# Kernel tuning notes

Measured on AMD Instinct MI355X. Metric: run time of the kernel, lower is better.

Reference implementation:

```python
import jax, jax.numpy as jnp
import numpy as np

B, N, T, D, E, M = 8, 512, 64, 128, 32, 3


def _norm(v):
    return v / jnp.clip(jnp.linalg.norm(v, axis=-1, keepdims=True), 1e-12)


def setup_inputs() -> dict:
    key = jax.random.key(0)
    ks = jax.random.split(key, 14)
    s = 0.05
    x = jax.random.normal(ks[0], (B, N, T, 1), jnp.float32)
    # set_prior: binarized adjacency + self loops, row-normalized
    a = (jax.random.uniform(ks[1], (N, N)) > 0.95).astype(jnp.float32) + jnp.eye(N, dtype=jnp.float32)
    prior = a / jnp.clip(a.sum(1, keepdims=True), 1e-8)
    # orthogonal queries, as in torch __init__ (QR of zero-padded randn)
    rng = np.random.default_rng(0)
    qs = []
    for _ in range(M):
        pad = np.zeros((D, D), np.float32)
        pad[:E] = rng.standard_normal((E, D)).astype(np.float32) * 0.1
        q, _ = np.linalg.qr(pad)
        qs.append(q[:E])
    return {
        "x": x,
        "prior": prior,
        "proj_W": jax.random.normal(ks[2], (D, 1), jnp.float32) * s,
        "proj_b": jnp.zeros((D,), jnp.float32),
        "W_ih": jax.random.normal(ks[3], (3 * D, D), jnp.float32) * s,
        "W_hh": jax.random.normal(ks[4], (3 * D, D), jnp.float32) * s,
        "b_ih": jnp.zeros((3 * D,), jnp.float32),
        "b_hh": jnp.zeros((3 * D,), jnp.float32),
        "space_W": jax.random.normal(ks[5], (M, D, D), jnp.float32) * s,
        "space_b": jnp.zeros((M, D), jnp.float32),
        "router_W": jax.random.normal(ks[6], (M, 2 * D), jnp.float32) * s,
        "router_b": jnp.zeros((M,), jnp.float32),
        "out_W": jax.random.normal(ks[7], (1, D), jnp.float32) * s,
        "out_b": jnp.zeros((1,), jnp.float32),
        "prior_logit": jnp.array(1.0, jnp.float32),
        "queries": jnp.asarray(np.stack(qs)),  # [M, E, D]
    }


def reference(x, prior, proj_W, proj_b, W_ih, W_hh, b_ih, b_hh,
              space_W, space_b, router_W, router_b, out_W, out_b,
              prior_logit, queries):
    b, n, t, _ = x.shape
    d = proj_b.shape[0]
    m, e, _ = queries.shape
    # proj(x.permute(0,2,1,3)).reshape(B*N, T, D)  (faithful reshape of [B,T,N,D])
    hp = jnp.transpose(x, (0, 2, 1, 3)) @ proj_W.T + proj_b  # [B,T,N,D]
    seq = hp.reshape(b * n, t, d)
    xs = jnp.swapaxes(seq, 0, 1)  # [T, BN, D]

    def gru_step(h, xt):
        gi = xt @ W_ih.T + b_ih
        gh = h @ W_hh.T + b_hh
        ir, iz, i_n = jnp.split(gi, 3, axis=-1)
        hr, hz, h_n = jnp.split(gh, 3, axis=-1)
        r = jax.nn.sigmoid(ir + hr)
        z = jax.nn.sigmoid(iz + hz)
        ng = jnp.tanh(i_n + r * h_n)
        return (1.0 - z) * ng + z * h, None

    h, _ = jax.lax.scan(gru_step, jnp.zeros((b * n, d), x.dtype), xs)
    h = h.reshape(b, n, d)

    stats = jnp.concatenate([h.mean(1), jnp.std(h, axis=1, ddof=1)], axis=-1)  # torch std is unbiased
    probs = jax.nn.softmax(stats @ router_W.T + router_b, axis=-1)  # [B,M]

    z_prior = jnp.einsum('ij,bjd->bid', prior, h)

    hs = _norm(jnp.einsum('bnd,mkd->bmnk', h, space_W) + space_b[None, :, None, :])  # [B,M,N,D]
    q = _norm(queries)  # [M,E,D]
    scores = jnp.einsum('bmnd,med->bmen', hs, q)  # [B,M,E,N] (topk over N axis)
    k = min(n, max(4, int(n * 0.05)))
    vals, idx = jax.lax.top_k(scores, k)  # [B,M,E,k]
    w = jax.nn.softmax(vals / 0.7, axis=-1)
    H = jnp.zeros((b, m, e, n), h.dtype).at[
        jnp.arange(b)[:, None, None, None],
        jnp.arange(m)[None, :, None, None],
        jnp.arange(e)[None, None, :, None],
        idx,
    ].set(w)  # [B,M,E,N], transposed layout of torch's [B,N,E]

    Hmix = jnp.einsum('bmen,bm->ben', H, probs)  # [B,E,N] == torch Hmix^T
    edge = jnp.einsum('ben,bnd->bed', Hmix, h)   # Hmix^T @ h
    z_learn = jnp.einsum('ben,bed->bnd', Hmix, edge)  # Hmix @ edge

    alpha = jax.nn.sigmoid(prior_logit)
    out = (alpha * z_prior + (1.0 - alpha) * z_learn) @ out_W.T + out_b  # [B,N,1]
    return out.squeeze(-1), probs
```

## Files before the change

kernel.cpp:

```cpp
#include <hip/hip_runtime.h>
#include <math.h>

#define OFF_U      0
#define OFF_C      384
#define OFF_QWHI   768
#define OFF_QWLO   6912
#define OFF_H      13056
#define OFF_PROBS  537344
#define OFF_HV     537376
#define OFF_SCORES 541472
#define OFF_HMIX   934688
#define OFF_WHI    1066016
#define OFF_SHI    1115168
#define OFF_SLO    1139744
#define OFF_STATS  1164320
#define OFF_EV     1229856
#define OFF_QB     1230112

typedef short bf16x8 __attribute__((ext_vector_type(8)));
typedef float f32x4 __attribute__((ext_vector_type(4)));

union U8 { unsigned short s[8]; bf16x8 v; uint4 u4; };

__device__ __forceinline__ unsigned short bf16_rtn(float f) {
  unsigned int u = __float_as_uint(f);
  return (unsigned short)((u + 0x7FFFu + ((u >> 16) & 1u)) >> 16);
}
__device__ __forceinline__ float bf16_f(unsigned short h) {
  return __uint_as_float(((unsigned int)h) << 16);
}

__global__ __launch_bounds__(256) void prep_kernel(const float* __restrict__ Wih,
                                                   const float* __restrict__ projW,
                                                   const float* __restrict__ projb,
                                                   const float* __restrict__ bih,
                                                   const float* __restrict__ queries,
                                                   const float* __restrict__ Whh,
                                                   const float* __restrict__ spaceW,
                                                   const float* __restrict__ spaceb,
                                                   float* __restrict__ ws) {
  const int bid = blockIdx.x, tid = threadIdx.x;
  const int wave = tid >> 6, lane = tid & 63;
  if (bid < 96) {
    int r = bid * 4 + wave;
    float w0 = Wih[r * 128 + lane], w1 = Wih[r * 128 + 64 + lane];
    float u = w0 * projW[lane] + w1 * projW[64 + lane];
    float c = w0 * projb[lane] + w1 * projb[64 + lane];
    for (int off = 32; off; off >>= 1) {
      u += __shfl_xor(u, off);
      c += __shfl_xor(c, off);
    }
    if (lane == 0) {
      ws[OFF_U + r] = u;
      ws[OFF_C + r] = c + bih[r];
    }
  } else if (bid < 112) {
    unsigned short* WHI = (unsigned short*)(ws + OFF_WHI);
    int base = (bid - 96) * 3072;
    for (int i = tid; i < 3072; i += 256)
      WHI[base + i] = bf16_rtn(Whh[base + i]);
  } else if (bid < 128) {
    unsigned short* SHI = (unsigned short*)(ws + OFF_SHI);
    unsigned short* SLO = (unsigned short*)(ws + OFF_SLO);
    int base = (bid - 112) * 3072;
    for (int i = tid; i < 3072; i += 256) {
      float w = spaceW[base + i];
      unsigned short hi = bf16_rtn(w);
      SHI[base + i] = hi;
      SLO[base + i] = bf16_rtn(w - bf16_f(hi));
    }
  } else if (bid < 224) {
    int qi = bid - 128;
    int m = qi >> 5, e = qi & 31;
    __shared__ float invS, qdS;
    const float* qrow = queries + (m * 32 + e) * 128;
    if (wave == 0) {
      float v0 = qrow[lane], v1 = qrow[64 + lane];
      float ss = v0 * v0 + v1 * v1;
      for (int off = 32; off; off >>= 1) ss += __shfl_xor(ss, off);
      if (lane == 0) invS = 1.f / fmaxf(sqrtf(ss), 1e-12f);
    } else if (wave == 1) {
      float v = qrow[lane] * spaceb[m * 128 + lane] +
                qrow[64 + lane] * spaceb[m * 128 + 64 + lane];
      for (int off = 32; off; off >>= 1) v += __shfl_xor(v, off);
      if (lane == 0) qdS = v;
    }
    __syncthreads();
    if (tid < 128) {
      int din = tid;
      float acc = 0.f;
      for (int dout = 0; dout < 128; ++dout)
        acc += qrow[dout] * spaceW[m * 16384 + dout * 128 + din];
      acc *= invS;
      unsigned short hi = bf16_rtn(acc);
      ((unsigned short*)(ws + OFF_QWHI))[(m * 32 + e) * 128 + din] = hi;
      ((unsigned short*)(ws + OFF_QWLO))[(m * 32 + e) * 128 + din] =
          bf16_rtn(acc - bf16_f(hi));
    }
    if (tid == 255) ws[OFF_QB + m * 32 + e] = qdS * invS;
  } else {
    ws[OFF_EV + tid] = 0.f;
  }
}

__global__ __launch_bounds__(512, 2) void gru_kernel(const float* __restrict__ x,
                                                     const float* __restrict__ bhh,
                                                     const float* __restrict__ outW,
                                                     float* __restrict__ ws) {
  __shared__ __align__(16) unsigned short hB[2][16 * 17 * 8];
  __shared__ float xsAll[16 * 65];
  __shared__ float hFin[16 * 132];

  const int tid = threadIdx.x, wave = tid >> 6, lane = tid & 63;
  const int q = lane >> 4, s15 = lane & 15;
  const int d = wave * 16 + s15;
  const unsigned short* WHI = (const unsigned short*)(ws + OFF_WHI);

  {
    float4 z4 = make_float4(0.f, 0.f, 0.f, 0.f);
    float4* hm4 = (float4*)(ws + OFF_HMIX);
    if (tid < 128) hm4[blockIdx.x * 128 + tid] = z4;
  }

  bf16x8 Bh[3][4];
#pragma unroll
  for (int t = 0; t < 3; ++t) {
    int row = (wave + 8 * t) * 16 + s15;
#pragma unroll
    for (int c = 0; c < 4; ++c)
      Bh[t][c] = *(const bf16x8*)&WHI[row * 128 + c * 32 + q * 8];
  }
  const float ur = ws[OFF_U + d],       uz = ws[OFF_U + 128 + d], un = ws[OFF_U + 256 + d];
  const float cr = ws[OFF_C + d] + bhh[d];
  const float cz = ws[OFF_C + 128 + d] + bhh[128 + d];
  const float cn = ws[OFF_C + 256 + d];
  const float bj2 = bhh[256 + d];

  const int seq0 = blockIdx.x * 16;
  for (int i = tid; i < 1024; i += 512) {
    int s = i >> 6, tt = i & 63;
    int r = (seq0 + s) * 64 + tt;
    xsAll[s * 65 + tt] = x[((r >> 15) * 512 + (r & 511)) * 64 + ((r >> 9) & 63)];
  }
  for (int i = tid; i < 2176; i += 512) hB[0][i] = 0;
  __syncthreads();

  float hreg[4] = {0.f, 0.f, 0.f, 0.f};
  const int g = d >> 3, e = d & 7;

  for (int t = 0; t < 64; ++t) {
    const int rb = t & 1, wb = rb ^ 1;
    f32x4 acc0 = {0.f, 0.f, 0.f, 0.f};
    f32x4 acc1 = {0.f, 0.f, 0.f, 0.f};
    f32x4 acc2 = {0.f, 0.f, 0.f, 0.f};
#pragma unroll
    for (int c = 0; c < 4; ++c) {
      bf16x8 A = *(const bf16x8*)&hB[rb][((c * 4 + q) * 17 + s15) * 8];
      acc0 = __builtin_amdgcn_mfma_f32_16x16x32_bf16(A, Bh[0][c], acc0, 0, 0, 0);
      acc1 = __builtin_amdgcn_mfma_f32_16x16x32_bf16(A, Bh[1][c], acc1, 0, 0, 0);
      acc2 = __builtin_amdgcn_mfma_f32_16x16x32_bf16(A, Bh[2][c], acc2, 0, 0, 0);
    }
    float xsv[4];
#pragma unroll
    for (int r = 0; r < 4; ++r) xsv[r] = xsAll[(q * 4 + r) * 65 + t];
#pragma unroll
    for (int r = 0; r < 4; ++r) {
      int s = q * 4 + r;
      float gr = fmaf(xsv[r], ur, cr + acc0[r]);
      float gz = fmaf(xsv[r], uz, cz + acc1[r]);
      float gn = fmaf(xsv[r], un, cn);
      float hn = acc2[r] + bj2;
      float rr = __builtin_amdgcn_rcpf(1.f + __expf(-gr));
      float zm = __builtin_amdgcn_rcpf(1.f + __expf(gz));
      float a = fmaf(rr, hn, gn);
      float ng = 1.f - 2.f * __builtin_amdgcn_rcpf(__expf(2.f * a) + 1.f);
      float hv = fmaf(zm, ng - hreg[r], hreg[r]);
      hreg[r] = hv;
      hB[wb][(g * 17 + s) * 8 + e] = bf16_rtn(hv);
    }
    __syncthreads();
  }

#pragma unroll
  for (int r = 0; r < 4; ++r) hFin[(q * 4 + r) * 132 + d] = hreg[r];
  __syncthreads();
  float* h_out = ws + OFF_H;
#pragma unroll
  for (int p = 0; p < 4; ++p) {
    int item = tid + p * 512;
    int s = item >> 7, dd = item & 127;
    h_out[(seq0 + s) * 128 + dd] = hFin[s * 132 + dd];
  }
  for (int s = wave * 2; s < wave * 2 + 2; ++s) {
    float a = hFin[s * 132 + lane] * outW[lane] + hFin[s * 132 + 64 + lane] * outW[64 + lane];
    for (int off = 32; off; off >>= 1) a += __shfl_xor(a, off);
    if (lane == 0) ws[OFF_HV + seq0 + s] = a;
  }
  if (tid < 128) {
    float s = 0.f, q2 = 0.f;
#pragma unroll
    for (int sI = 0; sI < 16; ++sI) {
      float v = hFin[sI * 132 + tid];
      s += v; q2 += v * v;
    }
    ws[OFF_STATS + blockIdx.x * 256 + tid] = s;
    ws[OFF_STATS + blockIdx.x * 256 + 128 + tid] = q2;
  }
}

__global__ __launch_bounds__(256) void scores_kernel(const float* __restrict__ spaceb,
                                                     const float* __restrict__ routerW,
                                                     const float* __restrict__ routerb,
                                                     float* __restrict__ ws,
                                                     float* __restrict__ d_out) {
  const int bid = blockIdx.x;
  const int chunk = bid & 15, m = (bid >> 4) % 3, b = bid / 48;
  const int n0 = chunk * 32;
  const int tid = threadIdx.x, wave = tid >> 6, lane = tid & 63;
  const int q = lane >> 4, s15 = lane & 15;

  __shared__ __align__(16) unsigned short sHi[16 * 33 * 8];
  __shared__ __align__(16) unsigned short sLo[16 * 33 * 8];
  __shared__ float hsL[32 * 132];
  __shared__ float biasL[128];
  __shared__ float invnL[32];
  __shared__ float qbL[32];

  const float* hG = ws + OFF_H;
  const unsigned short* SHI = (const unsigned short*)(ws + OFF_SHI);
  const unsigned short* SLO = (const unsigned short*)(ws + OFF_SLO);
  const unsigned short* QWHI = (const unsigned short*)(ws + OFF_QWHI);
  const unsigned short* QWLO = (const unsigned short*)(ws + OFF_QWLO);

  if (tid < 128) biasL[tid] = spaceb[m * 128 + tid];
  else if (tid < 160) qbL[tid - 128] = ws[OFF_QB + m * 32 + (tid - 128)];
  {
    int nn = tid >> 3, kc = tid & 7;
    const float* row = &hG[(b * 512 + n0 + nn) * 128 + kc * 16];
    U8 ph0, pl0, ph1, pl1;
#pragma unroll
    for (int j = 0; j < 8; ++j) {
      float v = row[j];
      unsigned short hi = bf16_rtn(v);
      ph0.s[j] = hi; pl0.s[j] = bf16_rtn(v - bf16_f(hi));
    }
#pragma unroll
    for (int j = 0; j < 8; ++j) {
      float v = row[8 + j];
      unsigned short hi = bf16_rtn(v);
      ph1.s[j] = hi; pl1.s[j] = bf16_rtn(v - bf16_f(hi));
    }
    int g0 = kc * 2;
    *(uint4*)&sHi[(g0 * 33 + nn) * 8] = ph0.u4;
    *(uint4*)&sLo[(g0 * 33 + nn) * 8] = pl0.u4;
    *(uint4*)&sHi[((g0 + 1) * 33 + nn) * 8] = ph1.u4;
    *(uint4*)&sLo[((g0 + 1) * 33 + nn) * 8] = pl1.u4;
  }
  __syncthreads();

  const int nt = wave >> 1;
  const int half = wave & 1;
  const int dt0 = half * 4;
  f32x4 acc[4] = {{0.f,0.f,0.f,0.f},{0.f,0.f,0.f,0.f},{0.f,0.f,0.f,0.f},{0.f,0.f,0.f,0.f}};
  f32x4 accS = {0.f, 0.f, 0.f, 0.f};
#pragma unroll
  for (int c = 0; c < 4; ++c) {
    bf16x8 Ahi = *(const bf16x8*)&sHi[((c * 4 + q) * 33 + nt * 16 + s15) * 8];
    bf16x8 Alo = *(const bf16x8*)&sLo[((c * 4 + q) * 33 + nt * 16 + s15) * 8];
#pragma unroll
    for (int i = 0; i < 4; ++i) {
      int row = m * 16384 + ((dt0 + i) * 16 + s15) * 128 + c * 32 + q * 8;
      bf16x8 Bhi = *(const bf16x8*)&SHI[row];
      bf16x8 Blo = *(const bf16x8*)&SLO[row];
      acc[i] = __builtin_amdgcn_mfma_f32_16x16x32_bf16(Ahi, Bhi, acc[i], 0, 0, 0);
      acc[i] = __builtin_amdgcn_mfma_f32_16x16x32_bf16(Alo, Bhi, acc[i], 0, 0, 0);
      acc[i] = __builtin_amdgcn_mfma_f32_16x16x32_bf16(Ahi, Blo, acc[i], 0, 0, 0);
    }
    {
      int row = (m * 32 + half * 16 + s15) * 128 + c * 32 + q * 8;
      bf16x8 Qhi = *(const bf16x8*)&QWHI[row];
      bf16x8 Qlo = *(const bf16x8*)&QWLO[row];
      accS = __builtin_amdgcn_mfma_f32_16x16x32_bf16(Ahi, Qhi, accS, 0, 0, 0);
      accS = __builtin_amdgcn_mfma_f32_16x16x32_bf16(Alo, Qhi, accS, 0, 0, 0);
      accS = __builtin_amdgcn_mfma_f32_16x16x32_bf16(Ahi, Qlo, accS, 0, 0, 0);
    }
  }
#pragma unroll
  for (int i = 0; i < 4; ++i) {
    int dcol = (dt0 + i) * 16 + s15;
    float bb = biasL[dcol];
#pragma unroll
    for (int r = 0; r < 4; ++r)
      hsL[(nt * 16 + q * 4 + r) * 132 + dcol] = acc[i][r] + bb;
  }
  __syncthreads();

  {
    int n = tid >> 3, kc = tid & 7;
    float ss = 0.f;
#pragma unroll
    for (int d4 = 0; d4 < 4; ++d4) {
      float4 v = *(const float4*)&hsL[n * 132 + kc * 16 + d4 * 4];
      ss += v.x * v.x + v.y * v.y + v.z * v.z + v.w * v.w;
    }
    ss += __shfl_xor(ss, 1); ss += __shfl_xor(ss, 2); ss += __shfl_xor(ss, 4);
    if (kc == 0) invnL[n] = 1.f / fmaxf(sqrtf(ss), 1e-12f);
  }
  __syncthreads();

  {
    int e = half * 16 + s15;
    float qb = qbL[e];
    int nb = nt * 16 + q * 4;
    float4 o;
    o.x = (accS[0] + qb) * invnL[nb + 0];
    o.y = (accS[1] + qb) * invnL[nb + 1];
    o.z = (accS[2] + qb) * invnL[nb + 2];
    o.w = (accS[3] + qb) * invnL[nb + 3];
    *(float4*)&ws[OFF_SCORES + ((b * 3 + m) * 32 + e) * 512 + n0 + nb] = o;
  }

  if ((bid % 48) == 0) {
    __syncthreads();
    float* st = hsL;
    float* lgS = hsL + 256;
    if (tid < 128) {
      float s = 0.f, q2 = 0.f;
      const float* base = ws + OFF_STATS + b * 32 * 256;
      for (int j = 0; j < 32; ++j) {
        s += base[j * 256 + tid];
        q2 += base[j * 256 + 128 + tid];
      }
      float mean = s * (1.f / 512.f);
      float var = (q2 - 512.f * mean * mean) * (1.f / 511.f);
      st[tid] = mean;
      st[128 + tid] = sqrtf(fmaxf(var, 0.f));
    }
    __syncthreads();
    if (tid < 3) {
      float acc2 = routerb[tid];
      for (int k = 0; k < 256; ++k) acc2 += st[k] * routerW[tid * 256 + k];
      lgS[tid] = acc2;
    }
    __syncthreads();
    if (tid == 0) {
      float mx = fmaxf(lgS[0], fmaxf(lgS[1], lgS[2]));
      float e0 = expf(lgS[0] - mx), e1 = expf(lgS[1] - mx), e2 = expf(lgS[2] - mx);
      float inv = 1.f / (e0 + e1 + e2);
      ws[OFF_PROBS + b * 3 + 0] = e0 * inv;
      ws[OFF_PROBS + b * 3 + 1] = e1 * inv;
      ws[OFF_PROBS + b * 3 + 2] = e2 * inv;
      d_out[4096 + b * 3 + 0] = e0 * inv;
      d_out[4096 + b * 3 + 1] = e1 * inv;
      d_out[4096 + b * 3 + 2] = e2 * inv;
    }
  }
}

__global__ __launch_bounds__(256) void topk_kernel(float* __restrict__ ws) {
  const int row0 = blockIdx.x * 4;
  const int b = row0 / 96;
  const int tid = threadIdx.x, wave = tid >> 6, lane = tid & 63;
  __shared__ float hvL[512];
  hvL[tid] = ws[OFF_HV + b * 512 + tid];
  hvL[256 + tid] = ws[OFF_HV + b * 512 + 256 + tid];
  __syncthreads();

  int row = row0 + wave;
  int m = (row / 32) % 3, e = row & 31;
  const float* sc = ws + OFF_SCORES + row * 512;
  float prob = ws[OFF_PROBS + b * 3 + m];

  float v[8];
#pragma unroll
  for (int j = 0; j < 8; ++j) v[j] = sc[j * 64 + lane];

  float selv = 0.f; int seli = 0; float maxv = 0.f;
  for (int it = 0; it < 25; ++it) {
    float bv = v[0]; int bj = 0;
#pragma unroll
    for (int j = 1; j < 8; ++j)
      if (v[j] > bv) { bv = v[j]; bj = j; }
    int bidx = bj * 64 + lane;
    for (int off = 32; off; off >>= 1) {
      float ov = __shfl_xor(bv, off);
      int oi = __shfl_xor(bidx, off);
      if (ov > bv || (ov == bv && oi < bidx)) { bv = ov; bidx = oi; }
    }
    if (lane == (bidx & 63)) v[bidx >> 6] = -INFINITY;
    if (it == 0) maxv = bv;
    if (lane == it) { selv = bv; seli = bidx; }
  }
  float ex = (lane < 25) ? __expf((selv - maxv) * (1.f / 0.7f)) : 0.f;
  float den = ex;
  for (int off = 32; off; off >>= 1) den += __shfl_xor(den, off);
  float w = prob * ex / den;
  if (lane < 25)
    atomicAdd(&ws[OFF_HMIX + (b * 32 + e) * 512 + seli], w);
  float evc = (lane < 25) ? w * hvL[seli] : 0.f;
  for (int off = 32; off; off >>= 1) evc += __shfl_xor(evc, off);
  if (lane == 0) atomicAdd(&ws[OFF_EV + b * 32 + e], evc);
}

__global__ __launch_bounds__(512) void final_kernel(const float* __restrict__ prior,
                                                    const float* __restrict__ outb,
                                                    const float* __restrict__ plog,
                                                    float* __restrict__ ws,
                                                    float* __restrict__ d_out) {
  const int bid = blockIdx.x;
  const int b = bid >> 4, ch = bid & 15;
  const int tid = threadIdx.x, wave = tid >> 6, lane = tid & 63;
  __shared__ float hvL[512], evL[32];
  hvL[tid] = ws[OFF_HV + b * 512 + tid];
  if (tid < 32) evL[tid] = ws[OFF_EV + b * 32 + tid];
  __syncthreads();
  float alpha = 1.f / (1.f + expf(-plog[0]));
  float ob = outb[0];
#pragma unroll
  for (int i = 0; i < 4; ++i) {
    int n = ch * 32 + wave * 4 + i;
    const float* pr = prior + n * 512;
    float s1 = 0.f;
#pragma unroll
    for (int j = 0; j < 8; ++j) s1 += pr[j * 64 + lane] * hvL[j * 64 + lane];
    float s2 = 0.f;
    if (lane < 32) s2 = ws[OFF_HMIX + (b * 32 + lane) * 512 + n] * evL[lane];
    float a = alpha * s1 + (1.f - alpha) * s2;
    for (int off = 32; off; off >>= 1) a += __shfl_xor(a, off);
    if (lane == 0) d_out[b * 512 + n] = a + ob;
  }
}

extern "C" void kernel_launch(void* const* d_in, const int* in_sizes, int n_in,
                              void* d_out, int out_size, void* d_ws, size_t ws_size,
                              hipStream_t stream) {
  const float* x       = (const float*)d_in[0];
  const float* prior   = (const float*)d_in[1];
  const float* projW   = (const float*)d_in[2];
  const float* projb   = (const float*)d_in[3];
  const float* Wih     = (const float*)d_in[4];
  const float* Whh     = (const float*)d_in[5];
  const float* bih     = (const float*)d_in[6];
  const float* bhh     = (const float*)d_in[7];
  const float* spaceW  = (const float*)d_in[8];
  const float* spaceb  = (const float*)d_in[9];
  const float* routerW = (const float*)d_in[10];
  const float* routerb = (const float*)d_in[11];
  const float* outW    = (const float*)d_in[12];
  const float* outb    = (const float*)d_in[13];
  const float* plog    = (const float*)d_in[14];
  const float* queries = (const float*)d_in[15];
  float* ws  = (float*)d_ws;
  float* out = (float*)d_out;

  prep_kernel<<<225, 256, 0, stream>>>(Wih, projW, projb, bih, queries, Whh,
                                       spaceW, spaceb, ws);
  gru_kernel<<<256, 512, 0, stream>>>(x, bhh, outW, ws);
  scores_kernel<<<384, 256, 0, stream>>>(spaceb, routerW, routerb, ws, out);
  topk_kernel<<<192, 256, 0, stream>>>(ws);
  final_kernel<<<128, 512, 0, stream>>>(prior, outb, plog, ws, out);
}
```

Measured before the change: 177.7 us.

## Transpose GRU MFMA operands, fold log2e into weights, pack bf16 stores

The GRU step now puts the recurrent weights in the A operand and the hidden state in the B operand. Each lane therefore owns four consecutive hidden dims of one sequence, and the x input is a single scalar per lane. The log2(e) scaling is folded into W_hh and the gate constants during prep, so the gates use raw exp2 and the biases start in the accumulator. New h values are packed with v_cvt_pk_bf16_f32 and written as one 8-byte LDS store. The loop is manually unrolled by two to make the buffer indices compile-time constants. Together these cut per-step VALU work, LDS store count and address arithmetic on the serial 64-step critical path. The cost is a slightly different rounding, since W_hh is scaled before the bf16 conversion.

After: 167.1 us. 6.0% less time.

```diff
diff --git a/kernel.cpp b/kernel.cpp
--- a/kernel.cpp
+++ b/kernel.cpp
@@ -16,6 +16,8 @@
 #define OFF_STATS  1164320
 #define OFF_EV     1229856
 #define OFF_QB     1230112
+
+#define L2E_F 1.44269504088896340736f
 
 typedef short bf16x8 __attribute__((ext_vector_type(8)));
 typedef float f32x4 __attribute__((ext_vector_type(4)));
@@ -57,8 +59,11 @@
   } else if (bid < 112) {
     unsigned short* WHI = (unsigned short*)(ws + OFF_WHI);
     int base = (bid - 96) * 3072;
-    for (int i = tid; i < 3072; i += 256)
-      WHI[base + i] = bf16_rtn(Whh[base + i]);
+    for (int i = tid; i < 3072; i += 256) {
+      int idx = base + i;
+      float sc = (idx < 32768) ? L2E_F : (2.f * L2E_F);
+      WHI[idx] = bf16_rtn(Whh[idx] * sc);
+    }
   } else if (bid < 128) {
     unsigned short* SHI = (unsigned short*)(ws + OFF_SHI);
     unsigned short* SLO = (unsigned short*)(ws + OFF_SLO);
@@ -103,17 +108,47 @@
   }
 }
 
+#define GRU_STEP(RB, WB, T)                                                         \
+  do {                                                                              \
+    f32x4 acc0 = c0i, acc1 = c1i, acc2 = c2i;                                       \
+    _Pragma("unroll") for (int c = 0; c < 4; ++c) {                                 \
+      bf16x8 Bf = *(const bf16x8*)&hB[RB][rdOff + c * 32];                          \
+      acc0 = __builtin_amdgcn_mfma_f32_16x16x32_bf16(Ah[0][c], Bf, acc0, 0, 0, 0);  \
+      acc1 = __builtin_amdgcn_mfma_f32_16x16x32_bf16(Ah[1][c], Bf, acc1, 0, 0, 0);  \
+      acc2 = __builtin_amdgcn_mfma_f32_16x16x32_bf16(Ah[2][c], Bf, acc2, 0, 0, 0);  \
+    }                                                                               \
+    const float xsv = xsAll[xsOff + (T)];                                           \
+    float hv[4];                                                                    \
+    _Pragma("unroll") for (int r = 0; r < 4; ++r) {                                 \
+      float gr = fmaf(xsv, ur[r], acc0[r]);                                         \
+      float gz = fmaf(xsv, uz[r], acc1[r]);                                         \
+      float gn = fmaf(xsv, un[r], cnv[r]);                                          \
+      float rr = __builtin_amdgcn_rcpf(1.f + __builtin_amdgcn_exp2f(-gr));          \
+      float zm = __builtin_amdgcn_rcpf(1.f + __builtin_amdgcn_exp2f(gz));           \
+      float a = fmaf(rr, acc2[r], gn);                                              \
+      float ng = fmaf(-2.f, __builtin_amdgcn_rcpf(__builtin_amdgcn_exp2f(a) + 1.f), \
+                      1.f);                                                         \
+      hv[r] = fmaf(zm, ng - hreg[r], hreg[r]);                                      \
+      hreg[r] = hv[r];                                                              \
+    }                                                                               \
+    unsigned int pk0, pk1;                                                          \
+    asm("v_cvt_pk_bf16_f32 %0, %1, %2" : "=v"(pk0) : "v"(hv[0]), "v"(hv[1]));       \
+    asm("v_cvt_pk_bf16_f32 %0, %1, %2" : "=v"(pk1) : "v"(hv[2]), "v"(hv[3]));       \
+    *(uint2*)&hB[WB][wrOff] = make_uint2(pk0, pk1);                                 \
+    __syncthreads();                                                                \
+  } while (0)
+
 __global__ __launch_bounds__(512, 2) void gru_kernel(const float* __restrict__ x,
                                                      const float* __restrict__ bhh,
                                                      const float* __restrict__ outW,
                                                      float* __restrict__ ws) {
-  __shared__ __align__(16) unsigned short hB[2][16 * 17 * 8];
+  __shared__ __align__(16) unsigned short hB[2][16 * 136];
   __shared__ float xsAll[16 * 65];
   __shared__ float hFin[16 * 132];
 
   const int tid = threadIdx.x, wave = tid >> 6, lane = tid & 63;
   const int q = lane >> 4, s15 = lane & 15;
-  const int d = wave * 16 + s15;
+  const int d0 = wave * 16 + q * 4;
   const unsigned short* WHI = (const unsigned short*)(ws + OFF_WHI);
 
   {
@@ -122,19 +157,28 @@
     if (tid < 128) hm4[blockIdx.x * 128 + tid] = z4;
   }
 
-  bf16x8 Bh[3][4];
+  bf16x8 Ah[3][4];
 #pragma unroll
   for (int t = 0; t < 3; ++t) {
     int row = (wave + 8 * t) * 16 + s15;
 #pragma unroll
     for (int c = 0; c < 4; ++c)
-      Bh[t][c] = *(const bf16x8*)&WHI[row * 128 + c * 32 + q * 8];
-  }
-  const float ur = ws[OFF_U + d],       uz = ws[OFF_U + 128 + d], un = ws[OFF_U + 256 + d];
-  const float cr = ws[OFF_C + d] + bhh[d];
-  const float cz = ws[OFF_C + 128 + d] + bhh[128 + d];
-  const float cn = ws[OFF_C + 256 + d];
-  const float bj2 = bhh[256 + d];
+      Ah[t][c] = *(const bf16x8*)&WHI[row * 128 + c * 32 + q * 8];
+  }
+
+  float ur[4], uz[4], un[4], cnv[4];
+  f32x4 c0i, c1i, c2i;
+#pragma unroll
+  for (int r = 0; r < 4; ++r) {
+    int d = d0 + r;
+    ur[r] = ws[OFF_U + d] * L2E_F;
+    uz[r] = ws[OFF_U + 128 + d] * L2E_F;
+    un[r] = ws[OFF_U + 256 + d] * (2.f * L2E_F);
+    c0i[r] = (ws[OFF_C + d] + bhh[d]) * L2E_F;
+    c1i[r] = (ws[OFF_C + 128 + d] + bhh[128 + d]) * L2E_F;
+    cnv[r] = ws[OFF_C + 256 + d] * (2.f * L2E_F);
+    c2i[r] = bhh[256 + d] * (2.f * L2E_F);
+  }
 
   const int seq0 = blockIdx.x * 16;
   for (int i = tid; i < 1024; i += 512) {
@@ -146,43 +190,18 @@
   __syncthreads();
 
   float hreg[4] = {0.f, 0.f, 0.f, 0.f};
-  const int g = d >> 3, e = d & 7;
-
-  for (int t = 0; t < 64; ++t) {
-    const int rb = t & 1, wb = rb ^ 1;
-    f32x4 acc0 = {0.f, 0.f, 0.f, 0.f};
-    f32x4 acc1 = {0.f, 0.f, 0.f, 0.f};
-    f32x4 acc2 = {0.f, 0.f, 0.f, 0.f};
-#pragma unroll
-    for (int c = 0; c < 4; ++c) {
-      bf16x8 A = *(const bf16x8*)&hB[rb][((c * 4 + q) * 17 + s15) * 8];
-      acc0 = __builtin_amdgcn_mfma_f32_16x16x32_bf16(A, Bh[0][c], acc0, 0, 0, 0);
-      acc1 = __builtin_amdgcn_mfma_f32_16x16x32_bf16(A, Bh[1][c], acc1, 0, 0, 0);
-      acc2 = __builtin_amdgcn_mfma_f32_16x16x32_bf16(A, Bh[2][c], acc2, 0, 0, 0);
-    }
-    float xsv[4];
-#pragma unroll
-    for (int r = 0; r < 4; ++r) xsv[r] = xsAll[(q * 4 + r) * 65 + t];
-#pragma unroll
-    for (int r = 0; r < 4; ++r) {
-      int s = q * 4 + r;
-      float gr = fmaf(xsv[r], ur, cr + acc0[r]);
-      float gz = fmaf(xsv[r], uz, cz + acc1[r]);
-      float gn = fmaf(xsv[r], un, cn);
-      float hn = acc2[r] + bj2;
-      float rr = __builtin_amdgcn_rcpf(1.f + __expf(-gr));
-      float zm = __builtin_amdgcn_rcpf(1.f + __expf(gz));
-      float a = fmaf(rr, hn, gn);
-      float ng = 1.f - 2.f * __builtin_amdgcn_rcpf(__expf(2.f * a) + 1.f);
-      float hv = fmaf(zm, ng - hreg[r], hreg[r]);
-      hreg[r] = hv;
-      hB[wb][(g * 17 + s) * 8 + e] = bf16_rtn(hv);
-    }
-    __syncthreads();
-  }
-
-#pragma unroll
-  for (int r = 0; r < 4; ++r) hFin[(q * 4 + r) * 132 + d] = hreg[r];
+  const int rdOff = s15 * 136 + q * 8;
+  const int wrOff = s15 * 136 + d0;
+  const int xsOff = s15 * 65;
+
+#pragma unroll 1
+  for (int t2 = 0; t2 < 32; ++t2) {
+    GRU_STEP(0, 1, 2 * t2);
+    GRU_STEP(1, 0, 2 * t2 + 1);
+  }
+
+#pragma unroll
+  for (int r = 0; r < 4; ++r) hFin[s15 * 132 + d0 + r] = hreg[r];
   __syncthreads();
   float* h_out = ws + OFF_H;
 #pragma unroll
```
